# Kernel tuning notes

Measured on AMD Instinct MI355X. Metric: run time of the kernel, lower is better.

## Reference

```python
import jax, jax.numpy as jnp
import numpy as np

B = 256                 # number of graphs (batch_size)
NODES_PER_GRAPH = 2000
N = B * NODES_PER_GRAPH # 512000 total nodes
F_IN = 64               # node_features
HID = 32                # DCRNN hidden size (hardcoded in module)
E = 2_000_000           # number of edges


def setup_inputs() -> dict:
    key = jax.random.key(0)
    ks = jax.random.split(key, 12)
    x = jax.random.normal(ks[0], (N, F_IN), jnp.float32)
    edge_index = jax.random.randint(ks[1], (2, E), 0, N, dtype=jnp.int64)
    edge_weight = jax.random.uniform(ks[2], (E,), jnp.float32)
    batch = jnp.repeat(jnp.arange(B, dtype=jnp.int64), NODES_PER_GRAPH)
    s = float(1.0 / np.sqrt(F_IN + HID))
    def dconv_w(k):
        return jax.random.uniform(k, (2, 1, F_IN + HID, HID), jnp.float32, -s, s)
    Wz, Wr, Wh = dconv_w(ks[3]), dconv_w(ks[4]), dconv_w(ks[5])
    bz = jax.random.uniform(ks[6], (HID,), jnp.float32, -s, s)
    br = jax.random.uniform(ks[7], (HID,), jnp.float32, -s, s)
    bh = jax.random.uniform(ks[8], (HID,), jnp.float32, -s, s)
    sl = float(1.0 / np.sqrt(HID))
    Wl = jax.random.uniform(ks[9], (1, HID), jnp.float32, -sl, sl)
    bl = jax.random.uniform(ks[10], (1,), jnp.float32, -sl, sl)
    return {"x": x, "edge_index": edge_index, "edge_weight": edge_weight,
            "batch": batch, "Wz": Wz, "bz": bz, "Wr": Wr, "br": br,
            "Wh": Wh, "bh": bh, "Wl": Wl, "bl": bl}


def reference(x, edge_index, edge_weight, batch, Wz, bz, Wr, br, Wh, bh, Wl, bl):
    # DConv with K=1: only the two order-0 diffusion terms contribute,
    # i.e. X @ W[0,0] + X @ W[1,0] + b (edge_index/edge_weight unused in math).
    def dconv(X, W, b):
        return X @ (W[0, 0] + W[1, 0]) + b

    n = x.shape[0]
    H0 = jnp.zeros((n, HID), x.dtype)           # initial hidden state
    XH = jnp.concatenate([x, H0], axis=1)       # [N, F_IN+HID]
    Z = jax.nn.sigmoid(dconv(XH, Wz, bz))       # update gate
    R = jax.nn.sigmoid(dconv(XH, Wr, br))       # reset gate
    Ht = jnp.tanh(dconv(jnp.concatenate([x, R * H0], axis=1), Wh, bh))
    H = Z * H0 + (1.0 - Z) * Ht                  # GRU-style state update

    h = jax.nn.relu(H)
    h = h @ Wl.T + bl                            # Linear(32 -> 1)

    # global_mean_pool: scatter-mean over graph ids
    sums = jax.ops.segment_sum(h, batch, num_segments=B)
    counts = jax.ops.segment_sum(jnp.ones((n,), h.dtype), batch, num_segments=B)
    return sums / jnp.maximum(counts, 1.0)[:, None]   # [B, 1]
```

## Files before the change

kernel.cpp:

```cpp
#include <hip/hip_runtime.h>
#include <math.h>

#define N_NODES   512000
#define F_IN      64
#define HID       32
#define B_GRAPHS  256
#define NPG       2000
#define CHUNKS_PER_GRAPH 8
#define NODES_PER_CHUNK  250


__global__ __launch_bounds__(256) void setup_kernel(
    const float* __restrict__ Wz, const float* __restrict__ bz,
    const float* __restrict__ Wh, const float* __restrict__ bh,
    const float* __restrict__ Wl, const float* __restrict__ bl,
    float* __restrict__ ws, float* __restrict__ out)
{
    int i = blockIdx.x * blockDim.x + threadIdx.x;
    if (i < 4096) {
        int k = i >> 6;
        int j = i & 63;
        float v;
        if (j < HID) {
            v = Wz[k * HID + j] + Wz[3072 + k * HID + j];
        } else {
            int jj = j - HID;
            v = Wh[k * HID + jj] + Wh[3072 + k * HID + jj];
        }
        ws[i] = v;
    }
    if (i < 64)       ws[4096 + i] = (i < HID) ? bz[i] : bh[i - HID];
    if (i < HID)      ws[4160 + i] = Wl[i];
    if (i == 0)       ws[4192] = bl[0];
    if (i < B_GRAPHS) out[i] = 0.f;
}

__global__ __launch_bounds__(256) void gcn_kernel(
    const float* __restrict__ x, const float* __restrict__ ws,
    float* __restrict__ out)
{
    const float* __restrict__ Wc = ws;
    const float* __restrict__ bb = ws + 4096;
    const float* __restrict__ Wl = ws + 4160;

    const int blk   = blockIdx.x;
    const int g     = blk >> 3;
    const int chunk = blk & 7;
    const int t     = threadIdx.x;

    float h = 0.f;
    if (t < NODES_PER_CHUNK) {
        const int n = g * NPG + chunk * NODES_PER_CHUNK + t;
        const float4* __restrict__ xr = (const float4*)(x + (size_t)n * F_IN);

        float acc[64];
        #pragma unroll
        for (int j = 0; j < 64; j++) acc[j] = 0.f;

        #pragma unroll 2
        for (int k4 = 0; k4 < 16; k4++) {
            const float4 xv = xr[k4];
            const float* __restrict__ w = Wc + (k4 * 4) * 64;
            #pragma unroll
            for (int j = 0; j < 64; j++) {
                float a = acc[j];
                a = fmaf(xv.x, w[j],        a);
                a = fmaf(xv.y, w[64  + j],  a);
                a = fmaf(xv.z, w[128 + j],  a);
                a = fmaf(xv.w, w[192 + j],  a);
                acc[j] = a;
            }
        }

        #pragma unroll
        for (int j = 0; j < HID; j++) {
            float zl = acc[j] + bb[j];
            float z  = 1.f / (1.f + __expf(-zl));
            float tl = acc[HID + j] + bb[HID + j];
            float e  = __expf(2.f * tl);
            float th = 1.f - 2.f / (e + 1.f);
            float H  = (1.f - z) * th;
            h = fmaf(fmaxf(H, 0.f), Wl[j], h);
        }
        h += ws[4192];
    }

    #pragma unroll
    for (int off = 32; off > 0; off >>= 1) h += __shfl_down(h, off);

    __shared__ float red[4];
    const int wid = t >> 6;
    if ((t & 63) == 0) red[wid] = h;
    __syncthreads();
    if (t == 0) {
        float s = red[0] + red[1] + red[2] + red[3];
        atomicAdd(&out[g], s * (1.0f / (float)NPG));
    }
}

extern "C" void kernel_launch(void* const* d_in, const int* in_sizes, int n_in,
                              void* d_out, int out_size, void* d_ws, size_t ws_size,
                              hipStream_t stream)
{
    const float* x  = (const float*)d_in[0];
    const float* Wz = (const float*)d_in[4];
    const float* bz = (const float*)d_in[5];
    const float* Wh = (const float*)d_in[8];
    const float* bh = (const float*)d_in[9];
    const float* Wl = (const float*)d_in[10];
    const float* bl = (const float*)d_in[11];
    float* out = (float*)d_out;
    float* ws  = (float*)d_ws;

    setup_kernel<<<16, 256, 0, stream>>>(Wz, bz, Wh, bh, Wl, bl, ws, out);
    gcn_kernel<<<B_GRAPHS * CHUNKS_PER_GRAPH, 256, 0, stream>>>(x, ws, out);
}
```

Before: 249.2 us.

## Map output columns to lanes with register-resident weights, loop nodes per wave

Restructures the GEMV so each of the 64 lanes owns one output column (32 z-gate, 32 candidate) and keeps its 64 weights in registers. Each wave walks 125 nodes, reading one broadcast x row per node. The gate nonlinearities become a single exp2/rcp per lane, and the z/tanh pair is combined via a cross-half shuffle. This removes the per-thread 64-float accumulators and the repeated weight loads. In exchange, each wave handles nodes serially with uniform x loads, which may limit memory-level parallelism, and every wave issues its own atomic.

```diff
diff --git a/kernel.cpp b/kernel.cpp
--- a/kernel.cpp
+++ b/kernel.cpp
@@ -6,8 +6,9 @@
 #define HID       32
 #define B_GRAPHS  256
 #define NPG       2000
-#define CHUNKS_PER_GRAPH 8
-#define NODES_PER_CHUNK  250
+#define NODES_PER_BLOCK 500
+#define NODES_PER_WAVE  125
+#define GRID_BLOCKS (N_NODES / NODES_PER_BLOCK)
 
 
 __global__ __launch_bounds__(256) void setup_kernel(
@@ -31,71 +32,56 @@
     }
     if (i < 64)       ws[4096 + i] = (i < HID) ? bz[i] : bh[i - HID];
     if (i < HID)      ws[4160 + i] = Wl[i];
-    if (i == 0)       ws[4192] = bl[0];
-    if (i < B_GRAPHS) out[i] = 0.f;
+    if (i < B_GRAPHS) out[i] = bl[0];
 }
 
 __global__ __launch_bounds__(256) void gcn_kernel(
     const float* __restrict__ x, const float* __restrict__ ws,
     float* __restrict__ out)
 {
-    const float* __restrict__ Wc = ws;
-    const float* __restrict__ bb = ws + 4096;
-    const float* __restrict__ Wl = ws + 4160;
+    const int lane = threadIdx.x & 63;
+    const int wid  = __builtin_amdgcn_readfirstlane(threadIdx.x >> 6);
+    const int blk  = blockIdx.x;
+    const int g    = blk >> 2;
 
-    const int blk   = blockIdx.x;
-    const int g     = blk >> 3;
-    const int chunk = blk & 7;
-    const int t     = threadIdx.x;
+    float Wk[64];
+    #pragma unroll
+    for (int k = 0; k < 64; k++) Wk[k] = ws[k * 64 + lane];
 
-    float h = 0.f;
-    if (t < NODES_PER_CHUNK) {
-        const int n = g * NPG + chunk * NODES_PER_CHUNK + t;
-        const float4* __restrict__ xr = (const float4*)(x + (size_t)n * F_IN);
+    const float bb_lane = ws[4096 + lane];
+    const float wl_lane = (lane < HID) ? ws[4160 + lane] : 0.f;
+    const float s2 = (lane < HID) ? -1.4426950408889634f : 2.8853900817779268f;
+    const float c0 = (lane < HID) ? 0.f : 1.f;
+    const float c1 = (lane < HID) ? 1.f : -2.f;
 
-        float acc[64];
+    const int base = blk * NODES_PER_BLOCK + wid * NODES_PER_WAVE;
+    const float4* __restrict__ xr = (const float4*)(x + (size_t)base * F_IN);
+
+    float hacc = 0.f;
+    for (int i = 0; i < NODES_PER_WAVE; i++) {
+        float a0 = 0.f, a1 = 0.f, a2 = 0.f, a3 = 0.f;
         #pragma unroll
-        for (int j = 0; j < 64; j++) acc[j] = 0.f;
-
-        #pragma unroll 2
         for (int k4 = 0; k4 < 16; k4++) {
             const float4 xv = xr[k4];
-            const float* __restrict__ w = Wc + (k4 * 4) * 64;
-            #pragma unroll
-            for (int j = 0; j < 64; j++) {
-                float a = acc[j];
-                a = fmaf(xv.x, w[j],        a);
-                a = fmaf(xv.y, w[64  + j],  a);
-                a = fmaf(xv.z, w[128 + j],  a);
-                a = fmaf(xv.w, w[192 + j],  a);
-                acc[j] = a;
-            }
+            a0 = fmaf(xv.x, Wk[4 * k4 + 0], a0);
+            a1 = fmaf(xv.y, Wk[4 * k4 + 1], a1);
+            a2 = fmaf(xv.z, Wk[4 * k4 + 2], a2);
+            a3 = fmaf(xv.w, Wk[4 * k4 + 3], a3);
         }
+        xr += 16;
 
-        #pragma unroll
-        for (int j = 0; j < HID; j++) {
-            float zl = acc[j] + bb[j];
-            float z  = 1.f / (1.f + __expf(-zl));
-            float tl = acc[HID + j] + bb[HID + j];
-            float e  = __expf(2.f * tl);
-            float th = 1.f - 2.f / (e + 1.f);
-            float H  = (1.f - z) * th;
-            h = fmaf(fmaxf(H, 0.f), Wl[j], h);
-        }
-        h += ws[4192];
+        const float a = ((a0 + a1) + (a2 + a3)) + bb_lane;
+        const float e = exp2f(a * s2);
+        const float r = __builtin_amdgcn_rcpf(1.f + e);
+        const float val = fmaf(c1, r, c0);
+        const float p = __shfl(val, lane ^ 32, 64);
+        const float H = fmaf(-val, p, p);
+        hacc = fmaf(fmaxf(H, 0.f), wl_lane, hacc);
     }
 
     #pragma unroll
-    for (int off = 32; off > 0; off >>= 1) h += __shfl_down(h, off);
-
-    __shared__ float red[4];
-    const int wid = t >> 6;
-    if ((t & 63) == 0) red[wid] = h;
-    __syncthreads();
-    if (t == 0) {
-        float s = red[0] + red[1] + red[2] + red[3];
-        atomicAdd(&out[g], s * (1.0f / (float)NPG));
-    }
+    for (int off = 32; off > 0; off >>= 1) hacc += __shfl_down(hacc, off, 64);
+    if (lane == 0) atomicAdd(&out[g], hacc * (1.f / (float)NPG));
 }
 
 extern "C" void kernel_launch(void* const* d_in, const int* in_sizes, int n_in,
@@ -113,5 +99,5 @@
     float* ws  = (float*)d_ws;
 
     setup_kernel<<<16, 256, 0, stream>>>(Wz, bz, Wh, bh, Wl, bl, ws, out);
-    gcn_kernel<<<B_GRAPHS * CHUNKS_PER_GRAPH, 256, 0, stream>>>(x, ws, out);
+    gcn_kernel<<<GRID_BLOCKS, 256, 0, stream>>>(x, ws, out);
 }
```

Measured after the change: 322.8 us. 1.3x slower.
